# Kernel optimization log

Hardware: AMD Instinct MI355X
Metric: run time of the kernel (lower is better)

The kernel has to match this reference:

```python
import jax, jax.numpy as jnp
import numpy as np

FACTOR = 1.0   # module's self.factor
EPS = 1e-6     # rmsnorm eps


def setup_inputs() -> dict:
    key = jax.random.key(0)
    k0, k1, k2, k3 = jax.random.split(key, 4)
    B, S = 4, 2048
    D_IN = D_STATE = D_OUT = 2048
    N_HEADS = 32
    HD = D_STATE // N_HEADS  # 64
    x = jax.random.normal(k0, (B, S, D_IN), jnp.float32)
    w_in = jax.random.normal(k1, (D_STATE, D_IN), jnp.float32) * 0.02
    b_in = jnp.zeros((D_STATE,), jnp.float32)
    state_weight = jax.random.normal(k2, (N_HEADS, HD, HD), jnp.float32) * 0.02
    norm_weight = jnp.ones((D_STATE,), jnp.float32)
    w_out = jax.random.normal(k3, (D_OUT, D_STATE), jnp.float32) * (0.02 / np.sqrt(2 * 24))
    return dict(x=x, w_in=w_in, b_in=b_in, state_weight=state_weight,
                norm_weight=norm_weight, w_out=w_out)


def _rnn_scan(xt, W):
    # xt: (B, S, N, H); W: (N, H, H)
    B, S, N, H = xt.shape

    def step(s, x_t):
        # s: (B, N, H) ; per-head linear recurrence with tanh nonlinearity
        s = jnp.tanh(jnp.einsum('bnh,nhk->bnk', s, W) + x_t)
        return s, s

    s0 = jnp.zeros((B, N, H), xt.dtype)
    _, states = jax.lax.scan(step, s0, jnp.swapaxes(xt, 0, 1))  # (S, B, N, H)
    return jnp.swapaxes(states, 0, 1)  # (B, S, N, H)


def reference(x, w_in, b_in, state_weight, norm_weight, w_out):
    B, S, _ = x.shape
    N, H, _ = state_weight.shape
    h = x @ w_in.T + b_in                      # input_projection: (B,S,state)
    h = h.reshape(B, S, N, H) * FACTOR
    W = state_weight * FACTOR
    states = _rnn_scan(h, W)                   # (B,S,N,H)
    y = states.reshape(B, S, N * H)
    # rmsnorm
    y = y * jax.lax.rsqrt(jnp.mean(y * y, axis=-1, keepdims=True) + EPS) * norm_weight
    return y @ w_out.T                         # output_projection (no bias)
```

## Files before the change

kernel.cpp:

```cpp
#include <hip/hip_runtime.h>
#include <hip/hip_bf16.h>
#include <cstdint>


typedef short bf16x8 __attribute__((ext_vector_type(8)));
typedef float f32x4 __attribute__((ext_vector_type(4)));
typedef float f32x2 __attribute__((ext_vector_type(2)));

#define GLD16(gp, lp)                                                          \
  __builtin_amdgcn_global_load_lds(                                            \
      (const __attribute__((address_space(1))) void*)(gp),                     \
      (__attribute__((address_space(3))) void*)(lp), 16, 0, 0)

__global__ __launch_bounds__(256) void cvt_f32_bf16(
    const float* __restrict__ in, __hip_bfloat16* __restrict__ out, int n4) {
  int i = blockIdx.x * 256 + threadIdx.x;
  if (i >= n4) return;
  float4 v = ((const float4*)in)[i];
  __hip_bfloat16 a = __float2bfloat16(v.x);
  __hip_bfloat16 b = __float2bfloat16(v.y);
  __hip_bfloat16 c = __float2bfloat16(v.z);
  __hip_bfloat16 d = __float2bfloat16(v.w);
  ushort4 p;
  p.x = *(unsigned short*)&a; p.y = *(unsigned short*)&b;
  p.z = *(unsigned short*)&c; p.w = *(unsigned short*)&d;
  ((ushort4*)out)[i] = p;
}

__global__ __launch_bounds__(256) void gemm_nt(
    const __hip_bfloat16* __restrict__ A, const __hip_bfloat16* __restrict__ B,
    const float* __restrict__ bias, float* __restrict__ C,
    int M, int N, int K) {
  __shared__ __hip_bfloat16 As[128 * 32];
  __shared__ __hip_bfloat16 Bs[128 * 32];
  const int tid  = threadIdx.x;
  const int lane = tid & 63;
  const int wave = tid >> 6;
  const int wm = wave >> 1, wn = wave & 1;
  const long bm = (long)blockIdx.y * 128;
  const long bn = (long)blockIdx.x * 128;

  const int c0 = tid, c1 = tid + 256;
  const int r0 = c0 >> 2, k0 = (c0 & 3) * 8;
  const int r1 = c1 >> 2, k1 = (c1 & 3) * 8;
  __hip_bfloat16* lA0 = &As[(wave * 64) * 8];
  __hip_bfloat16* lA1 = &As[(256 + wave * 64) * 8];
  __hip_bfloat16* lB0 = &Bs[(wave * 64) * 8];
  __hip_bfloat16* lB1 = &Bs[(256 + wave * 64) * 8];
  const __hip_bfloat16* gA0 = A + (bm + r0) * (long)K + k0;
  const __hip_bfloat16* gA1 = A + (bm + r1) * (long)K + k1;
  const __hip_bfloat16* gB0 = B + (bn + r0) * (long)K + k0;
  const __hip_bfloat16* gB1 = B + (bn + r1) * (long)K + k1;

  const int fr = lane & 15;
  const int fk = (lane >> 4) * 8;

  f32x4 acc[4][4];
#pragma unroll
  for (int i = 0; i < 4; i++)
#pragma unroll
    for (int j = 0; j < 4; j++) acc[i][j] = {0.f, 0.f, 0.f, 0.f};

  for (int kt = 0; kt < K; kt += 32) {
    __syncthreads();
    GLD16(gA0 + kt, lA0);
    GLD16(gA1 + kt, lA1);
    GLD16(gB0 + kt, lB0);
    GLD16(gB1 + kt, lB1);
    __syncthreads();
    bf16x8 af[4], bfr[4];
#pragma unroll
    for (int t = 0; t < 4; t++)
      af[t] = *(const bf16x8*)&As[(wm * 64 + t * 16 + fr) * 32 + fk];
#pragma unroll
    for (int t = 0; t < 4; t++)
      bfr[t] = *(const bf16x8*)&Bs[(wn * 64 + t * 16 + fr) * 32 + fk];
#pragma unroll
    for (int i = 0; i < 4; i++)
#pragma unroll
      for (int j = 0; j < 4; j++)
        acc[i][j] = __builtin_amdgcn_mfma_f32_16x16x32_bf16(
            af[i], bfr[j], acc[i][j], 0, 0, 0);
  }

  const int cr = (lane >> 4) * 4;
  const int cc = lane & 15;
#pragma unroll
  for (int j = 0; j < 4; j++) {
    const long n = bn + wn * 64 + j * 16 + cc;
    const float bv = bias ? bias[n] : 0.0f;
#pragma unroll
    for (int i = 0; i < 4; i++) {
      const long m = bm + wm * 64 + i * 16 + cr;
#pragma unroll
      for (int r = 0; r < 4; r++)
        C[(m + r) * (long)N + n] = acc[i][j][r] + bv;
    }
  }
}

__device__ __forceinline__ void pk_fma(f32x2& d, f32x2 a, f32x2 b) {
  asm("v_pk_fma_f32 %0, %1, %2, %0" : "+v"(d) : "v"(a), "v"(b));
}

__device__ __forceinline__ float tanh_fast(float z) {
  float e = __expf(2.0f * z);
  return 1.0f - 2.0f * __builtin_amdgcn_rcpf(e + 1.0f);
}

__global__ __launch_bounds__(64) void scan_kernel(
    const float* __restrict__ Wst, float* __restrict__ h) {
  const int b = blockIdx.x >> 5;
  const int n = blockIdx.x & 31;
  const int lane = threadIdx.x;
  const float* Wn = Wst + n * 4096;
  f32x2 w2[32];
#pragma unroll
  for (int j = 0; j < 32; j++) {
    f32x2 t;
    t.x = Wn[(2 * j) * 64 + lane];
    t.y = Wn[(2 * j + 1) * 64 + lane];
    w2[j] = t;
  }

  __shared__ float s_lds[64];

  float4 sv[16];
#pragma unroll
  for (int i = 0; i < 16; i++) sv[i] = make_float4(0.f, 0.f, 0.f, 0.f);

  float* hp = h + ((size_t)b * 2048) * 2048 + n * 64 + lane;
  float xcur[8], xnxt[8];
#pragma unroll
  for (int i = 0; i < 8; i++) xcur[i] = hp[(size_t)i * 2048];

  for (int t0 = 0; t0 < 2048; t0 += 8) {
    if (t0 + 8 < 2048) {
#pragma unroll
      for (int i = 0; i < 8; i++)
        xnxt[i] = hp[(size_t)(t0 + 8 + i) * 2048];
    }
#pragma unroll
    for (int i = 0; i < 8; i++) {
      f32x2 acc[4];
      acc[0].x = xcur[i]; acc[0].y = 0.f;
      acc[1] = acc[2] = acc[3] = f32x2{0.f, 0.f};
#pragma unroll
      for (int q = 0; q < 16; q++) {
        f32x2 lo; lo.x = sv[q].x; lo.y = sv[q].y;
        f32x2 hi; hi.x = sv[q].z; hi.y = sv[q].w;
        pk_fma(acc[(2 * q) & 3], lo, w2[2 * q]);
        pk_fma(acc[(2 * q + 1) & 3], hi, w2[2 * q + 1]);
      }
      f32x2 s01 = acc[0] + acc[1];
      f32x2 s23 = acc[2] + acc[3];
      f32x2 st = s01 + s23;
      float sn = tanh_fast(st.x + st.y);
      s_lds[lane] = sn;
#pragma unroll
      for (int q = 0; q < 16; q++) sv[q] = ((const float4*)s_lds)[q];
      hp[(size_t)(t0 + i) * 2048] = sn;
    }
#pragma unroll
    for (int i = 0; i < 8; i++) xcur[i] = xnxt[i];
  }
}

__global__ __launch_bounds__(256) void rmsnorm_to_bf16(
    const float* __restrict__ Y, const float* __restrict__ g,
    __hip_bfloat16* __restrict__ O) {
  const long row = blockIdx.x;
  const float* yr = Y + row * 2048;
  const int tid = threadIdx.x;
  float4 v0 = ((const float4*)yr)[tid * 2];
  float4 v1 = ((const float4*)yr)[tid * 2 + 1];
  float ss = v0.x * v0.x + v0.y * v0.y + v0.z * v0.z + v0.w * v0.w +
             v1.x * v1.x + v1.y * v1.y + v1.z * v1.z + v1.w * v1.w;
#pragma unroll
  for (int off = 32; off > 0; off >>= 1) ss += __shfl_down(ss, off);
  __shared__ float red[4];
  if ((tid & 63) == 0) red[tid >> 6] = ss;
  __syncthreads();
  float inv = rsqrtf((red[0] + red[1] + red[2] + red[3]) * (1.0f / 2048.0f)
                     + 1e-6f);
  float4 g0 = ((const float4*)(g + tid * 8))[0];
  float4 g1 = ((const float4*)(g + tid * 8))[1];
  float ov[8] = {v0.x * inv * g0.x, v0.y * inv * g0.y,
                 v0.z * inv * g0.z, v0.w * inv * g0.w,
                 v1.x * inv * g1.x, v1.y * inv * g1.y,
                 v1.z * inv * g1.z, v1.w * inv * g1.w};
  ushort4 p0, p1;
  __hip_bfloat16 t;
  t = __float2bfloat16(ov[0]); p0.x = *(unsigned short*)&t;
  t = __float2bfloat16(ov[1]); p0.y = *(unsigned short*)&t;
  t = __float2bfloat16(ov[2]); p0.z = *(unsigned short*)&t;
  t = __float2bfloat16(ov[3]); p0.w = *(unsigned short*)&t;
  t = __float2bfloat16(ov[4]); p1.x = *(unsigned short*)&t;
  t = __float2bfloat16(ov[5]); p1.y = *(unsigned short*)&t;
  t = __float2bfloat16(ov[6]); p1.z = *(unsigned short*)&t;
  t = __float2bfloat16(ov[7]); p1.w = *(unsigned short*)&t;
  ushort4* op = (ushort4*)(O + row * 2048 + tid * 8);
  op[0] = p0;
  op[1] = p1;
}

extern "C" void kernel_launch(void* const* d_in, const int* in_sizes, int n_in,
                              void* d_out, int out_size, void* d_ws,
                              size_t ws_size, hipStream_t stream) {
  const float* x     = (const float*)d_in[0];
  const float* w_in  = (const float*)d_in[1];
  const float* b_in  = (const float*)d_in[2];
  const float* w_st  = (const float*)d_in[3];
  const float* nw    = (const float*)d_in[4];
  const float* w_out = (const float*)d_in[5];
  float* out = (float*)d_out;

  char* ws = (char*)d_ws;
  __hip_bfloat16* x_bf  = (__hip_bfloat16*)(ws);
  __hip_bfloat16* wi_bf = (__hip_bfloat16*)(ws + 33554432);
  __hip_bfloat16* wo_bf = (__hip_bfloat16*)(ws + 41943040);
  float* h              = (float*)(ws + 50331648);

  cvt_f32_bf16<<<16384, 256, 0, stream>>>(x, x_bf, 4194304);
  cvt_f32_bf16<<<4096, 256, 0, stream>>>(w_in, wi_bf, 1048576);
  cvt_f32_bf16<<<4096, 256, 0, stream>>>(w_out, wo_bf, 1048576);

  gemm_nt<<<dim3(16, 64), 256, 0, stream>>>(x_bf, wi_bf, b_in, h,
                                            8192, 2048, 2048);
  scan_kernel<<<128, 64, 0, stream>>>(w_st, h);
  rmsnorm_to_bf16<<<8192, 256, 0, stream>>>(h, nw, x_bf);
  gemm_nt<<<dim3(16, 64), 256, 0, stream>>>(x_bf, wo_bf, nullptr, out,
                                            8192, 2048, 2048);
}
```

Measured before the change: 794.1 us.

## Interleave two batch recurrences per scan wavefront to hide serial latency

Each scan block now handles two batch elements for the same head, sharing the per-head weight registers and interleaving the two independent FMA chains, tanh and LDS exchanges. The grid is halved from 128 to 64 blocks. The goal is to fill the latency of the serial dependent chain (FMA, tanh, LDS round-trip) with independent work. It also replaces expf with a direct exp2 builtin in tanh. The cost is higher register pressure and half as many concurrent waves on a GPU that was already mostly idle during the scan.

```diff
diff --git a/kernel.cpp b/kernel.cpp
--- a/kernel.cpp
+++ b/kernel.cpp
@@ -104,14 +104,15 @@
 }
 
 __device__ __forceinline__ float tanh_fast(float z) {
-  float e = __expf(2.0f * z);
+  float e = __builtin_amdgcn_exp2f(z * 2.8853900817779268f);
   return 1.0f - 2.0f * __builtin_amdgcn_rcpf(e + 1.0f);
 }
 
 __global__ __launch_bounds__(64) void scan_kernel(
     const float* __restrict__ Wst, float* __restrict__ h) {
-  const int b = blockIdx.x >> 5;
-  const int n = blockIdx.x & 31;
+  const int p  = blockIdx.x;
+  const int n  = p & 31;
+  const int bp = p >> 5;
   const int lane = threadIdx.x;
   const float* Wn = Wst + n * 4096;
   f32x2 w2[32];
@@ -123,46 +124,70 @@
     w2[j] = t;
   }
 
-  __shared__ float s_lds[64];
-
-  float4 sv[16];
-#pragma unroll
-  for (int i = 0; i < 16; i++) sv[i] = make_float4(0.f, 0.f, 0.f, 0.f);
-
-  float* hp = h + ((size_t)b * 2048) * 2048 + n * 64 + lane;
-  float xcur[8], xnxt[8];
-#pragma unroll
-  for (int i = 0; i < 8; i++) xcur[i] = hp[(size_t)i * 2048];
+  __shared__ float s_lds[128];
+
+  float4 svA[16], svB[16];
+#pragma unroll
+  for (int i = 0; i < 16; i++) {
+    svA[i] = make_float4(0.f, 0.f, 0.f, 0.f);
+    svB[i] = make_float4(0.f, 0.f, 0.f, 0.f);
+  }
+
+  float* hpA = h + ((size_t)(2 * bp) * 2048) * 2048 + n * 64 + lane;
+  float* hpB = hpA + (size_t)2048 * 2048;
+  float xcA[8], xnA[8], xcB[8], xnB[8];
+#pragma unroll
+  for (int i = 0; i < 8; i++) {
+    xcA[i] = hpA[(size_t)i * 2048];
+    xcB[i] = hpB[(size_t)i * 2048];
+  }
 
   for (int t0 = 0; t0 < 2048; t0 += 8) {
     if (t0 + 8 < 2048) {
 #pragma unroll
-      for (int i = 0; i < 8; i++)
-        xnxt[i] = hp[(size_t)(t0 + 8 + i) * 2048];
+      for (int i = 0; i < 8; i++) {
+        xnA[i] = hpA[(size_t)(t0 + 8 + i) * 2048];
+        xnB[i] = hpB[(size_t)(t0 + 8 + i) * 2048];
+      }
     }
 #pragma unroll
     for (int i = 0; i < 8; i++) {
-      f32x2 acc[4];
-      acc[0].x = xcur[i]; acc[0].y = 0.f;
-      acc[1] = acc[2] = acc[3] = f32x2{0.f, 0.f};
+      f32x2 aA[4], aB[4];
+      aA[0].x = xcA[i]; aA[0].y = 0.f;
+      aA[1] = aA[2] = aA[3] = f32x2{0.f, 0.f};
+      aB[0].x = xcB[i]; aB[0].y = 0.f;
+      aB[1] = aB[2] = aB[3] = f32x2{0.f, 0.f};
 #pragma unroll
       for (int q = 0; q < 16; q++) {
-        f32x2 lo; lo.x = sv[q].x; lo.y = sv[q].y;
-        f32x2 hi; hi.x = sv[q].z; hi.y = sv[q].w;
-        pk_fma(acc[(2 * q) & 3], lo, w2[2 * q]);
-        pk_fma(acc[(2 * q + 1) & 3], hi, w2[2 * q + 1]);
+        f32x2 loA; loA.x = svA[q].x; loA.y = svA[q].y;
+        f32x2 hiA; hiA.x = svA[q].z; hiA.y = svA[q].w;
+        f32x2 loB; loB.x = svB[q].x; loB.y = svB[q].y;
+        f32x2 hiB; hiB.x = svB[q].z; hiB.y = svB[q].w;
+        pk_fma(aA[(2 * q) & 3], loA, w2[2 * q]);
+        pk_fma(aB[(2 * q) & 3], loB, w2[2 * q]);
+        pk_fma(aA[(2 * q + 1) & 3], hiA, w2[2 * q + 1]);
+        pk_fma(aB[(2 * q + 1) & 3], hiB, w2[2 * q + 1]);
       }
-      f32x2 s01 = acc[0] + acc[1];
-      f32x2 s23 = acc[2] + acc[3];
-      f32x2 st = s01 + s23;
-      float sn = tanh_fast(st.x + st.y);
-      s_lds[lane] = sn;
-#pragma unroll
-      for (int q = 0; q < 16; q++) sv[q] = ((const float4*)s_lds)[q];
-      hp[(size_t)(t0 + i) * 2048] = sn;
+      f32x2 sA01 = aA[0] + aA[1];
+      f32x2 sA23 = aA[2] + aA[3];
+      f32x2 sAt = sA01 + sA23;
+      float snA = tanh_fast(sAt.x + sAt.y);
+      f32x2 sB01 = aB[0] + aB[1];
+      f32x2 sB23 = aB[2] + aB[3];
+      f32x2 sBt = sB01 + sB23;
+      float snB = tanh_fast(sBt.x + sBt.y);
+      s_lds[lane] = snA;
+      s_lds[64 + lane] = snB;
+#pragma unroll
+      for (int q = 0; q < 16; q++) {
+        svA[q] = ((const float4*)s_lds)[q];
+        svB[q] = ((const float4*)s_lds)[16 + q];
+      }
+      hpA[(size_t)(t0 + i) * 2048] = snA;
+      hpB[(size_t)(t0 + i) * 2048] = snB;
     }
 #pragma unroll
-    for (int i = 0; i < 8; i++) xcur[i] = xnxt[i];
+    for (int i = 0; i < 8; i++) { xcA[i] = xnA[i]; xcB[i] = xnB[i]; }
   }
 }
 
@@ -227,7 +252,7 @@
 
   gemm_nt<<<dim3(16, 64), 256, 0, stream>>>(x_bf, wi_bf, b_in, h,
                                             8192, 2048, 2048);
-  scan_kernel<<<128, 64, 0, stream>>>(w_st, h);
+  scan_kernel<<<64, 64, 0, stream>>>(w_st, h);
   rmsnorm_to_bf16<<<8192, 256, 0, stream>>>(h, nw, x_bf);
   gemm_nt<<<dim3(16, 64), 256, 0, stream>>>(x_bf, wo_bf, nullptr, out,
                                             8192, 2048, 2048);
```

Measured after the change: 1.094 ms. 37.7% more time.
